# Kernel optimization log

Measured on AMD Instinct MI355X. Metric: run time of the kernel, lower is better.

Reference implementation:

```python
import jax, jax.numpy as jnp
import numpy as np

DIM = 1024
HEADS = 16
DIM_HEAD = 64
INNER = HEADS * DIM_HEAD
LN_EPS = 1e-5


def setup_inputs() -> dict:
    key = jax.random.key(0)
    ks = jax.random.split(key, 6)
    b, n = 2, 2048
    x = jax.random.normal(ks[0], (b, n, DIM), dtype=jnp.float32)
    attn_bias = jax.random.normal(ks[1], (HEADS, n, n), dtype=jnp.float32)
    # learned params
    ln_gamma = jnp.ones((DIM,), dtype=jnp.float32)
    ln_beta = jnp.zeros((DIM,), dtype=jnp.float32)
    w_qkv = jax.random.normal(ks[2], (DIM, 3 * INNER), dtype=jnp.float32) / np.sqrt(DIM)
    w_out = jax.random.normal(ks[3], (INNER, DIM), dtype=jnp.float32) / np.sqrt(INNER)
    return {"x": x, "attn_bias": attn_bias, "ln_gamma": ln_gamma,
            "ln_beta": ln_beta, "w_qkv": w_qkv, "w_out": w_out}


def reference(x, attn_bias, ln_gamma, ln_beta, w_qkv, w_out):
    b, n, _ = x.shape
    scale = DIM_HEAD ** -0.5
    # LayerNorm
    mu = jnp.mean(x, axis=-1, keepdims=True)
    var = jnp.mean(jnp.square(x - mu), axis=-1, keepdims=True)
    xn = (x - mu) * jax.lax.rsqrt(var + LN_EPS) * ln_gamma + ln_beta
    # QKV projection: [b, n, 3*inner]
    qkv = xn @ w_qkv
    q, k, v = jnp.split(qkv, 3, axis=-1)
    # [b, n, inner] -> [b, h, n, d]
    split_heads = lambda t: t.reshape(b, n, HEADS, DIM_HEAD).transpose(0, 2, 1, 3)
    q, k, v = split_heads(q) * scale, split_heads(k), split_heads(v)
    sim = jnp.einsum('bhid,bhjd->bhij', q, k)
    sim = sim + attn_bias[None]  # broadcast over batch
    mask_value = -jnp.finfo(sim.dtype).max
    causal = jnp.triu(jnp.ones((n, n), dtype=bool), k=1)
    sim = jnp.where(causal, mask_value, sim)
    attn = jax.nn.softmax(sim, axis=-1)
    out = jnp.einsum('bhij,bhjd->bhid', attn, v)
    out = out.transpose(0, 2, 1, 3).reshape(b, n, INNER)
    return out @ w_out
```

## Files before the change

kernel.cpp:

```cpp
#include <hip/hip_runtime.h>
#include <hip/hip_bf16.h>
#include <math.h>

typedef unsigned short u16;
typedef __attribute__((ext_vector_type(8))) __bf16 bf16x8;
typedef __attribute__((ext_vector_type(4))) float f32x4;

static __device__ __forceinline__ u16 f2bf(float f) {
    unsigned int u = __builtin_bit_cast(unsigned int, f);
    u += 0x7fffu + ((u >> 16) & 1u);
    return (u16)(u >> 16);
}

__global__ __launch_bounds__(256) void ln_kernel(
    const float* __restrict__ x, const float* __restrict__ g,
    const float* __restrict__ bta, u16* __restrict__ xn)
{
    const int row = blockIdx.x;
    const int tid = threadIdx.x;
    const float4 v = *(const float4*)&x[(size_t)row * 1024 + tid * 4];
    float s  = v.x + v.y + v.z + v.w;
    float s2 = v.x * v.x + v.y * v.y + v.z * v.z + v.w * v.w;
    #pragma unroll
    for (int off = 32; off; off >>= 1) {
        s  += __shfl_xor(s,  off);
        s2 += __shfl_xor(s2, off);
    }
    __shared__ float red[8];
    if ((tid & 63) == 0) { red[tid >> 6] = s; red[4 + (tid >> 6)] = s2; }
    __syncthreads();
    s  = red[0] + red[1] + red[2] + red[3];
    s2 = red[4] + red[5] + red[6] + red[7];
    const float mean = s * (1.0f / 1024.0f);
    const float var  = s2 * (1.0f / 1024.0f) - mean * mean;
    const float rstd = rsqrtf(var + 1e-5f);
    const float4 gg = *(const float4*)&g[tid * 4];
    const float4 bb = *(const float4*)&bta[tid * 4];
    ushort4 o;
    o.x = f2bf((v.x - mean) * rstd * gg.x + bb.x);
    o.y = f2bf((v.y - mean) * rstd * gg.y + bb.y);
    o.z = f2bf((v.z - mean) * rstd * gg.z + bb.z);
    o.w = f2bf((v.w - mean) * rstd * gg.w + bb.w);
    *(ushort4*)&xn[(size_t)row * 1024 + tid * 4] = o;
}

__global__ __launch_bounds__(256) void transpose_w(
    const float* __restrict__ in, u16* __restrict__ outT, int K, int N)
{
    const int k0 = blockIdx.x * 64, n0 = blockIdx.y * 64;
    const int tid = threadIdx.x;
    __shared__ u16 tile[64][72];
    #pragma unroll
    for (int i = 0; i < 4; ++i) {
        int c = tid + i * 256;
        int kr = c >> 4, nc = (c & 15) * 4;
        float4 v = *(const float4*)&in[(size_t)(k0 + kr) * N + n0 + nc];
        tile[nc + 0][kr] = f2bf(v.x);
        tile[nc + 1][kr] = f2bf(v.y);
        tile[nc + 2][kr] = f2bf(v.z);
        tile[nc + 3][kr] = f2bf(v.w);
    }
    __syncthreads();
    #pragma unroll
    for (int i = 0; i < 4; ++i) {
        int c = tid + i * 256;
        int nr = c >> 4, kc = (c & 15) * 4;
        ushort4 w = *(const ushort4*)&tile[nr][kc];
        *(ushort4*)&outT[(size_t)(n0 + nr) * K + k0 + kc] = w;
    }
}

__global__ __launch_bounds__(256) void transpose_v_kernel(
    const u16* __restrict__ V, u16* __restrict__ Vt)
{
    const int bh = blockIdx.y;
    const int n0 = blockIdx.x * 64;
    const int tid = threadIdx.x;
    __shared__ u16 t[64][72];
    #pragma unroll
    for (int i = 0; i < 2; ++i) {
        int c = tid + (i << 8);
        int nr = c >> 3, dc = (c & 7) * 8;
        int4 v4 = *(const int4*)&V[((size_t)bh * 2048 + n0 + nr) * 64 + dc];
        union { int4 v; u16 u[8]; } uu; uu.v = v4;
        #pragma unroll
        for (int j = 0; j < 8; ++j) t[dc + j][nr] = uu.u[j];
    }
    __syncthreads();
    #pragma unroll
    for (int i = 0; i < 2; ++i) {
        int c = tid + (i << 8);
        int d = c >> 3, nn = (c & 7) * 8;
        int4 v4 = *(const int4*)&t[d][nn];
        *(int4*)&Vt[((size_t)bh * 64 + d) * 2048 + n0 + nn] = v4;
    }
}

template <int EPI>
__global__ __launch_bounds__(256) void gemm_bf16_k(
    const u16* __restrict__ A, const u16* __restrict__ Bt,
    int M, int N, int K,
    float* __restrict__ Cf,
    u16* __restrict__ Qo, u16* __restrict__ Ko, u16* __restrict__ Vo)
{
    __shared__ u16 lds[2][8192];
    const int tid = threadIdx.x;
    const int lane = tid & 63, w = tid >> 6;
    const int l15 = lane & 15, l4 = lane >> 4;
    const int wm = w & 1, wn = w >> 1;
    const int n0 = blockIdx.x * 128, m0 = blockIdx.y * 128;

    auto stage = [&](int buf, int kt) {
        const u16* Ab = A + (size_t)m0 * K + kt * 32;
        const u16* Bb = Bt + (size_t)n0 * K + kt * 32;
        #pragma unroll
        for (int i = 0; i < 2; ++i) {
            int c = tid + (i << 8);
            int r = c >> 2, ke = (c & 3) * 8;
            __builtin_amdgcn_global_load_lds(
                (const __attribute__((address_space(1))) void*)(Ab + (size_t)r * K + ke),
                (__attribute__((address_space(3))) void*)(&lds[buf][0] + c * 8), 16, 0, 0);
            __builtin_amdgcn_global_load_lds(
                (const __attribute__((address_space(1))) void*)(Bb + (size_t)r * K + ke),
                (__attribute__((address_space(3))) void*)(&lds[buf][4096] + c * 8), 16, 0, 0);
        }
    };

    f32x4 acc[4][4];
    #pragma unroll
    for (int mf = 0; mf < 4; ++mf)
        #pragma unroll
        for (int nf = 0; nf < 4; ++nf)
            acc[mf][nf] = f32x4{0.f, 0.f, 0.f, 0.f};

    const int NT = K >> 5;
    stage(0, 0);
    __syncthreads();
    for (int kt = 0; kt < NT; ++kt) {
        const int buf = kt & 1;
        if (kt + 1 < NT) stage(buf ^ 1, kt + 1);
        const u16* Ab = &lds[buf][0];
        const u16* Bb = &lds[buf][4096];
        bf16x8 af[4], bfv[4];
        #pragma unroll
        for (int mf = 0; mf < 4; ++mf)
            af[mf] = *(const bf16x8*)(Ab + (wm * 64 + mf * 16 + l15) * 32 + l4 * 8);
        #pragma unroll
        for (int nf = 0; nf < 4; ++nf)
            bfv[nf] = *(const bf16x8*)(Bb + (wn * 64 + nf * 16 + l15) * 32 + l4 * 8);
        #pragma unroll
        for (int mf = 0; mf < 4; ++mf)
            #pragma unroll
            for (int nf = 0; nf < 4; ++nf)
                acc[mf][nf] = __builtin_amdgcn_mfma_f32_16x16x32_bf16(
                    af[mf], bfv[nf], acc[mf][nf], 0, 0, 0);
        __syncthreads();
    }

    #pragma unroll
    for (int mf = 0; mf < 4; ++mf) {
        #pragma unroll
        for (int nf = 0; nf < 4; ++nf) {
            #pragma unroll
            for (int r = 0; r < 4; ++r) {
                const int row = m0 + wm * 64 + mf * 16 + l4 * 4 + r;
                const int col = n0 + wn * 64 + nf * 16 + l15;
                const float v = acc[mf][nf][r];
                if (EPI == 1) {
                    Cf[(size_t)row * N + col] = v;
                } else {
                    const int t = col >> 10, rem = col & 1023;
                    const int h = rem >> 6, d = rem & 63;
                    const int b = row >> 11, nn = row & 2047;
                    const size_t idx = ((size_t)((b * 16 + h) * 2048 + nn)) * 64 + d;
                    if (t == 0)      Qo[idx] = f2bf(v * 0.125f);
                    else if (t == 1) Ko[idx] = f2bf(v);
                    else             Vo[idx] = f2bf(v);
                }
            }
        }
    }
}

__global__ __launch_bounds__(512, 4) void attn_kernel(
    const u16* __restrict__ Q, const u16* __restrict__ Kmat,
    const u16* __restrict__ Vt, const float* __restrict__ bias,
    u16* __restrict__ att)
{
    const int hb = blockIdx.x;
    const int h = hb >> 1, b = hb & 1;
    const int bh = b * 16 + h;
    const int y = blockIdx.y;
    const int qb = (y < 8) ? y : 23 - y;
    const int q0 = qb << 7;
    const int tid = threadIdx.x;
    const int w = tid >> 6, lane = tid & 63;
    const int l15 = lane & 15, l4 = lane >> 4;

    __shared__ u16 K_lds[2][64][76];
    __shared__ u16 V_lds[2][64][76];
    __shared__ u16 P_lds[8][16][76];

    const int qrow = q0 + w * 16 + l15;
    const int qlim = q0 + w * 16 + 15;

    bf16x8 qa[2];
    #pragma unroll
    for (int ks = 0; ks < 2; ++ks)
        qa[ks] = *(const bf16x8*)(Q + ((size_t)bh * 2048 + qrow) * 64 + ks * 32 + l4 * 8);

    f32x4 acc[4];
    #pragma unroll
    for (int nf = 0; nf < 4; ++nf) acc[nf] = f32x4{0.f, 0.f, 0.f, 0.f};
    float m_r = -INFINITY, l_r = 0.f;

    const float* biasq = bias + (size_t)h * 2048 * 2048 + (size_t)qrow * 2048;

    const int rr_s = tid >> 3, pp_s = (tid & 7) * 8;
    int4 kreg, vreg;
    auto issue_loads = [&](int j0n) {
        kreg = *(const int4*)&Kmat[((size_t)bh * 2048 + j0n + rr_s) * 64 + pp_s];
        vreg = *(const int4*)&Vt[((size_t)bh * 64 + rr_s) * 2048 + j0n + pp_s];
    };
    auto load_bias = [&](int j0n, float4 (&dst)[4]) {
        #pragma unroll
        for (int nf = 0; nf < 4; ++nf)
            dst[nf] = *(const float4*)&biasq[j0n + nf * 16 + l4 * 4];
    };

    const int NT = 2 * qb + 2;
    float4 bregA[4], bregB[4];

    issue_loads(0);
    load_bias(0, bregA);
    if (64 <= qlim && NT > 1) load_bias(64, bregB);

    auto tile_step = [&](int jt, float4 (&bcur)[4]) {
        const int j0 = jt << 6;
        const int buf = jt & 1;
        *(int4*)&K_lds[buf][rr_s][pp_s] = kreg;
        *(int4*)&V_lds[buf][rr_s][pp_s] = vreg;
        if (jt + 1 < NT) issue_loads((jt + 1) << 6);
        __builtin_amdgcn_sched_barrier(0);
        asm volatile("s_waitcnt lgkmcnt(0)" ::: "memory");
        __builtin_amdgcn_s_barrier();
        __builtin_amdgcn_sched_barrier(0);

        if (j0 <= qlim) {
            f32x4 s[4];
            #pragma unroll
            for (int nf = 0; nf < 4; ++nf) s[nf] = f32x4{0.f, 0.f, 0.f, 0.f};
            __builtin_amdgcn_s_setprio(1);
            #pragma unroll
            for (int ks = 0; ks < 2; ++ks)
                #pragma unroll
                for (int nf = 0; nf < 4; ++nf) {
                    bf16x8 kb = *(const bf16x8*)&K_lds[buf][nf * 16 + l15][ks * 32 + l4 * 8];
                    s[nf] = __builtin_amdgcn_mfma_f32_16x16x32_bf16(kb, qa[ks], s[nf], 0, 0, 0);
                }
            __builtin_amdgcn_s_setprio(0);

            if (j0 + 63 > q0 + w * 16) {
                #pragma unroll
                for (int nf = 0; nf < 4; ++nf) {
                    const int col0 = j0 + nf * 16 + l4 * 4;
                    #pragma unroll
                    for (int r = 0; r < 4; ++r) {
                        const float v = s[nf][r] + ((const float*)&bcur[nf])[r];
                        s[nf][r] = (col0 + r > qrow) ? -1e30f : v;
                    }
                }
            } else {
                #pragma unroll
                for (int nf = 0; nf < 4; ++nf)
                    #pragma unroll
                    for (int r = 0; r < 4; ++r)
                        s[nf][r] += ((const float*)&bcur[nf])[r];
            }
            if (jt + 2 < NT && ((jt + 2) << 6) <= qlim)
                load_bias((jt + 2) << 6, bcur);

            float mt = fmaxf(fmaxf(fmaxf(s[0][0], s[0][1]), fmaxf(s[0][2], s[0][3])),
                             fmaxf(fmaxf(s[1][0], s[1][1]), fmaxf(s[1][2], s[1][3])));
            mt = fmaxf(mt, fmaxf(fmaxf(fmaxf(s[2][0], s[2][1]), fmaxf(s[2][2], s[2][3])),
                                 fmaxf(fmaxf(s[3][0], s[3][1]), fmaxf(s[3][2], s[3][3]))));
            mt = fmaxf(mt, __shfl_xor(mt, 16));
            mt = fmaxf(mt, __shfl_xor(mt, 32));
            if (__any(mt > m_r + 8.0f)) {
                const float mn = fmaxf(m_r, mt);
                const float alpha = __expf(m_r - mn);
                m_r = mn;
                l_r *= alpha;
                #pragma unroll
                for (int nf = 0; nf < 4; ++nf)
                    #pragma unroll
                    for (int r = 0; r < 4; ++r) acc[nf][r] *= alpha;
            }

            float ps = 0.f;
            #pragma unroll
            for (int nf = 0; nf < 4; ++nf) {
                union { ushort4 v; u16 e[4]; } pw;
                #pragma unroll
                for (int r = 0; r < 4; ++r) {
                    const float e = __expf(s[nf][r] - m_r);
                    ps += e;
                    pw.e[r] = f2bf(e);
                }
                *(ushort4*)&P_lds[w][l15][nf * 16 + l4 * 4] = pw.v;
            }
            ps += __shfl_xor(ps, 16);
            ps += __shfl_xor(ps, 32);
            l_r += ps;

            __builtin_amdgcn_s_setprio(1);
            #pragma unroll
            for (int ks = 0; ks < 2; ++ks) {
                bf16x8 pa = *(const bf16x8*)&P_lds[w][l15][ks * 32 + l4 * 8];
                #pragma unroll
                for (int nf = 0; nf < 4; ++nf) {
                    bf16x8 vb = *(const bf16x8*)&V_lds[buf][nf * 16 + l15][ks * 32 + l4 * 8];
                    acc[nf] = __builtin_amdgcn_mfma_f32_16x16x32_bf16(vb, pa, acc[nf], 0, 0, 0);
                }
            }
            __builtin_amdgcn_s_setprio(0);
        }
    };

    for (int jt = 0; jt < NT; jt += 2) {
        tile_step(jt,     bregA);
        tile_step(jt + 1, bregB);
    }

    const float inv = 1.0f / l_r;
    #pragma unroll
    for (int nf = 0; nf < 4; ++nf) {
        union { ushort4 v; u16 e[4]; } o;
        #pragma unroll
        for (int r = 0; r < 4; ++r) o.e[r] = f2bf(acc[nf][r] * inv);
        *(ushort4*)&att[((size_t)b * 2048 + qrow) * 1024 + h * 64 + nf * 16 + l4 * 4] = o.v;
    }
}

extern "C" void kernel_launch(void* const* d_in, const int* in_sizes, int n_in,
                              void* d_out, int out_size, void* d_ws, size_t ws_size,
                              hipStream_t stream) {
    const float* x     = (const float*)d_in[0];
    const float* bias  = (const float*)d_in[1];
    const float* gamma = (const float*)d_in[2];
    const float* beta_ = (const float*)d_in[3];
    const float* wqkv  = (const float*)d_in[4];
    const float* wout  = (const float*)d_in[5];
    float* out = (float*)d_out;

    char* ws = (char*)d_ws;
    u16* xn     = (u16*)(ws + 0);
    u16* wqkvT  = (u16*)(ws + 8388608);
    u16* woutT  = (u16*)(ws + 14680064);
    u16* Qb     = (u16*)(ws + 16777216);
    u16* Kb     = (u16*)(ws + 25165824);
    u16* Vb     = (u16*)(ws + 33554432);
    u16* Vtb    = (u16*)(ws + 41943040);
    u16* attb   = xn;

    ln_kernel<<<4096, 256, 0, stream>>>(x, gamma, beta_, xn);
    transpose_w<<<dim3(16, 48), 256, 0, stream>>>(wqkv, wqkvT, 1024, 3072);
    transpose_w<<<dim3(16, 16), 256, 0, stream>>>(wout, woutT, 1024, 1024);
    gemm_bf16_k<0><<<dim3(24, 32), 256, 0, stream>>>(xn, wqkvT, 4096, 3072, 1024,
                                                     nullptr, Qb, Kb, Vb);
    transpose_v_kernel<<<dim3(32, 32), 256, 0, stream>>>(Vb, Vtb);
    attn_kernel<<<dim3(32, 16), 512, 0, stream>>>(Qb, Kb, Vtb, bias, attb);
    gemm_bf16_k<1><<<dim3(8, 32), 256, 0, stream>>>(attb, woutT, 4096, 1024, 1024,
                                                    out, nullptr, nullptr, nullptr);
}
```

Before: 151.5 us.

## Merge prep kernels, write V transposed from QKV GEMM, deepen K/V prefetch

Folds LayerNorm and both weight transposes into one prep kernel launch. The QKV GEMM epilogue now writes V directly in transposed layout as 4-element vector stores, which removes the separate V transpose kernel and its extra round trip through memory. The attention kernel double-buffers the K/V register prefetch two tiles ahead to hide more global load latency. The costs are more live registers in attention and strided scattered stores in the GEMM epilogue.

```diff
diff --git a/kernel.cpp b/kernel.cpp
--- a/kernel.cpp
+++ b/kernel.cpp
@@ -12,87 +12,65 @@
     return (u16)(u >> 16);
 }
 
-__global__ __launch_bounds__(256) void ln_kernel(
+__global__ __launch_bounds__(256) void prep_kernel(
     const float* __restrict__ x, const float* __restrict__ g,
-    const float* __restrict__ bta, u16* __restrict__ xn)
+    const float* __restrict__ bta, u16* __restrict__ xn,
+    const float* __restrict__ wqkv, u16* __restrict__ wqkvT,
+    const float* __restrict__ wout, u16* __restrict__ woutT)
 {
-    const int row = blockIdx.x;
+    const int bid = blockIdx.x;
     const int tid = threadIdx.x;
-    const float4 v = *(const float4*)&x[(size_t)row * 1024 + tid * 4];
-    float s  = v.x + v.y + v.z + v.w;
-    float s2 = v.x * v.x + v.y * v.y + v.z * v.z + v.w * v.w;
-    #pragma unroll
-    for (int off = 32; off; off >>= 1) {
-        s  += __shfl_xor(s,  off);
-        s2 += __shfl_xor(s2, off);
-    }
-    __shared__ float red[8];
-    if ((tid & 63) == 0) { red[tid >> 6] = s; red[4 + (tid >> 6)] = s2; }
-    __syncthreads();
-    s  = red[0] + red[1] + red[2] + red[3];
-    s2 = red[4] + red[5] + red[6] + red[7];
-    const float mean = s * (1.0f / 1024.0f);
-    const float var  = s2 * (1.0f / 1024.0f) - mean * mean;
-    const float rstd = rsqrtf(var + 1e-5f);
-    const float4 gg = *(const float4*)&g[tid * 4];
-    const float4 bb = *(const float4*)&bta[tid * 4];
-    ushort4 o;
-    o.x = f2bf((v.x - mean) * rstd * gg.x + bb.x);
-    o.y = f2bf((v.y - mean) * rstd * gg.y + bb.y);
-    o.z = f2bf((v.z - mean) * rstd * gg.z + bb.z);
-    o.w = f2bf((v.w - mean) * rstd * gg.w + bb.w);
-    *(ushort4*)&xn[(size_t)row * 1024 + tid * 4] = o;
-}
-
-__global__ __launch_bounds__(256) void transpose_w(
-    const float* __restrict__ in, u16* __restrict__ outT, int K, int N)
-{
-    const int k0 = blockIdx.x * 64, n0 = blockIdx.y * 64;
-    const int tid = threadIdx.x;
-    __shared__ u16 tile[64][72];
-    #pragma unroll
-    for (int i = 0; i < 4; ++i) {
-        int c = tid + i * 256;
-        int kr = c >> 4, nc = (c & 15) * 4;
-        float4 v = *(const float4*)&in[(size_t)(k0 + kr) * N + n0 + nc];
-        tile[nc + 0][kr] = f2bf(v.x);
-        tile[nc + 1][kr] = f2bf(v.y);
-        tile[nc + 2][kr] = f2bf(v.z);
-        tile[nc + 3][kr] = f2bf(v.w);
-    }
-    __syncthreads();
-    #pragma unroll
-    for (int i = 0; i < 4; ++i) {
-        int c = tid + i * 256;
-        int nr = c >> 4, kc = (c & 15) * 4;
-        ushort4 w = *(const ushort4*)&tile[nr][kc];
-        *(ushort4*)&outT[(size_t)(n0 + nr) * K + k0 + kc] = w;
-    }
-}
-
-__global__ __launch_bounds__(256) void transpose_v_kernel(
-    const u16* __restrict__ V, u16* __restrict__ Vt)
-{
-    const int bh = blockIdx.y;
-    const int n0 = blockIdx.x * 64;
-    const int tid = threadIdx.x;
-    __shared__ u16 t[64][72];
-    #pragma unroll
-    for (int i = 0; i < 2; ++i) {
-        int c = tid + (i << 8);
-        int nr = c >> 3, dc = (c & 7) * 8;
-        int4 v4 = *(const int4*)&V[((size_t)bh * 2048 + n0 + nr) * 64 + dc];
-        union { int4 v; u16 u[8]; } uu; uu.v = v4;
-        #pragma unroll
-        for (int j = 0; j < 8; ++j) t[dc + j][nr] = uu.u[j];
-    }
-    __syncthreads();
-    #pragma unroll
-    for (int i = 0; i < 2; ++i) {
-        int c = tid + (i << 8);
-        int d = c >> 3, nn = (c & 7) * 8;
-        int4 v4 = *(const int4*)&t[d][nn];
-        *(int4*)&Vt[((size_t)bh * 64 + d) * 2048 + n0 + nn] = v4;
+    if (bid < 4096) {
+        const int row = bid;
+        const float4 v = *(const float4*)&x[(size_t)row * 1024 + tid * 4];
+        float s  = v.x + v.y + v.z + v.w;
+        float s2 = v.x * v.x + v.y * v.y + v.z * v.z + v.w * v.w;
+        #pragma unroll
+        for (int off = 32; off; off >>= 1) {
+            s  += __shfl_xor(s,  off);
+            s2 += __shfl_xor(s2, off);
+        }
+        __shared__ float red[8];
+        if ((tid & 63) == 0) { red[tid >> 6] = s; red[4 + (tid >> 6)] = s2; }
+        __syncthreads();
+        s  = red[0] + red[1] + red[2] + red[3];
+        s2 = red[4] + red[5] + red[6] + red[7];
+        const float mean = s * (1.0f / 1024.0f);
+        const float var  = s2 * (1.0f / 1024.0f) - mean * mean;
+        const float rstd = rsqrtf(var + 1e-5f);
+        const float4 gg = *(const float4*)&g[tid * 4];
+        const float4 bb = *(const float4*)&bta[tid * 4];
+        ushort4 o;
+        o.x = f2bf((v.x - mean) * rstd * gg.x + bb.x);
+        o.y = f2bf((v.y - mean) * rstd * gg.y + bb.y);
+        o.z = f2bf((v.z - mean) * rstd * gg.z + bb.z);
+        o.w = f2bf((v.w - mean) * rstd * gg.w + bb.w);
+        *(ushort4*)&xn[(size_t)row * 1024 + tid * 4] = o;
+    } else {
+        const float* in; u16* outT; int N, idx;
+        if (bid < 4864) { in = wqkv; outT = wqkvT; N = 3072; idx = bid - 4096; }
+        else            { in = wout; outT = woutT; N = 1024; idx = bid - 4864; }
+        const int K = 1024;
+        const int k0 = (idx & 15) * 64, n0 = (idx >> 4) * 64;
+        __shared__ u16 tile[64][72];
+        #pragma unroll
+        for (int i = 0; i < 4; ++i) {
+            int c = tid + i * 256;
+            int kr = c >> 4, nc = (c & 15) * 4;
+            float4 v = *(const float4*)&in[(size_t)(k0 + kr) * N + n0 + nc];
+            tile[nc + 0][kr] = f2bf(v.x);
+            tile[nc + 1][kr] = f2bf(v.y);
+            tile[nc + 2][kr] = f2bf(v.z);
+            tile[nc + 3][kr] = f2bf(v.w);
+        }
+        __syncthreads();
+        #pragma unroll
+        for (int i = 0; i < 4; ++i) {
+            int c = tid + i * 256;
+            int nr = c >> 4, kc = (c & 15) * 4;
+            ushort4 w = *(const ushort4*)&tile[nr][kc];
+            *(ushort4*)&outT[(size_t)(n0 + nr) * K + k0 + kc] = w;
+        }
     }
 }
 
@@ -101,7 +79,7 @@
     const u16* __restrict__ A, const u16* __restrict__ Bt,
     int M, int N, int K,
     float* __restrict__ Cf,
-    u16* __restrict__ Qo, u16* __restrict__ Ko, u16* __restrict__ Vo)
+    u16* __restrict__ Qo, u16* __restrict__ Ko, u16* __restrict__ Vto)
 {
     __shared__ u16 lds[2][8192];
     const int tid = threadIdx.x;
@@ -161,21 +139,28 @@
     for (int mf = 0; mf < 4; ++mf) {
         #pragma unroll
         for (int nf = 0; nf < 4; ++nf) {
-            #pragma unroll
-            for (int r = 0; r < 4; ++r) {
-                const int row = m0 + wm * 64 + mf * 16 + l4 * 4 + r;
-                const int col = n0 + wn * 64 + nf * 16 + l15;
-                const float v = acc[mf][nf][r];
-                if (EPI == 1) {
-                    Cf[(size_t)row * N + col] = v;
+            const int row0 = m0 + wm * 64 + mf * 16 + l4 * 4;
+            const int col  = n0 + wn * 64 + nf * 16 + l15;
+            if (EPI == 1) {
+                #pragma unroll
+                for (int r = 0; r < 4; ++r)
+                    Cf[(size_t)(row0 + r) * N + col] = acc[mf][nf][r];
+            } else {
+                const int t = col >> 10, rem = col & 1023;
+                const int h = rem >> 6, d = rem & 63;
+                const int b0 = row0 >> 11, nn0 = row0 & 2047;
+                if (t == 2) {
+                    union { ushort4 v; u16 e[4]; } vv;
+                    #pragma unroll
+                    for (int r = 0; r < 4; ++r) vv.e[r] = f2bf(acc[mf][nf][r]);
+                    *(ushort4*)&Vto[((size_t)((b0 * 16 + h) * 64) + d) * 2048 + nn0] = vv.v;
                 } else {
-                    const int t = col >> 10, rem = col & 1023;
-                    const int h = rem >> 6, d = rem & 63;
-                    const int b = row >> 11, nn = row & 2047;
-                    const size_t idx = ((size_t)((b * 16 + h) * 2048 + nn)) * 64 + d;
-                    if (t == 0)      Qo[idx] = f2bf(v * 0.125f);
-                    else if (t == 1) Ko[idx] = f2bf(v);
-                    else             Vo[idx] = f2bf(v);
+                    #pragma unroll
+                    for (int r = 0; r < 4; ++r) {
+                        const size_t idx = ((size_t)((b0 * 16 + h) * 2048 + nn0 + r)) * 64 + d;
+                        if (t == 0) Qo[idx] = f2bf(acc[mf][nf][r] * 0.125f);
+                        else        Ko[idx] = f2bf(acc[mf][nf][r]);
+                    }
                 }
             }
         }
@@ -217,10 +202,9 @@
     const float* biasq = bias + (size_t)h * 2048 * 2048 + (size_t)qrow * 2048;
 
     const int rr_s = tid >> 3, pp_s = (tid & 7) * 8;
-    int4 kreg, vreg;
-    auto issue_loads = [&](int j0n) {
-        kreg = *(const int4*)&Kmat[((size_t)bh * 2048 + j0n + rr_s) * 64 + pp_s];
-        vreg = *(const int4*)&Vt[((size_t)bh * 64 + rr_s) * 2048 + j0n + pp_s];
+    auto issue_k = [&](int j0n, int4& kd, int4& vd) {
+        kd = *(const int4*)&Kmat[((size_t)bh * 2048 + j0n + rr_s) * 64 + pp_s];
+        vd = *(const int4*)&Vt[((size_t)bh * 64 + rr_s) * 2048 + j0n + pp_s];
     };
     auto load_bias = [&](int j0n, float4 (&dst)[4]) {
         #pragma unroll
@@ -229,18 +213,20 @@
     };
 
     const int NT = 2 * qb + 2;
+    int4 kA, vA, kB, vB;
     float4 bregA[4], bregB[4];
 
-    issue_loads(0);
+    issue_k(0, kA, vA);
+    issue_k(64, kB, vB);
     load_bias(0, bregA);
-    if (64 <= qlim && NT > 1) load_bias(64, bregB);
-
-    auto tile_step = [&](int jt, float4 (&bcur)[4]) {
+    if (64 <= qlim) load_bias(64, bregB);
+
+    auto tile_step = [&](int jt, int4& kcur, int4& vcur, float4 (&bcur)[4]) {
         const int j0 = jt << 6;
         const int buf = jt & 1;
-        *(int4*)&K_lds[buf][rr_s][pp_s] = kreg;
-        *(int4*)&V_lds[buf][rr_s][pp_s] = vreg;
-        if (jt + 1 < NT) issue_loads((jt + 1) << 6);
+        *(int4*)&K_lds[buf][rr_s][pp_s] = kcur;
+        *(int4*)&V_lds[buf][rr_s][pp_s] = vcur;
+        if (jt + 2 < NT) issue_k((jt + 2) << 6, kcur, vcur);
         __builtin_amdgcn_sched_barrier(0);
         asm volatile("s_waitcnt lgkmcnt(0)" ::: "memory");
         __builtin_amdgcn_s_barrier();
@@ -328,8 +314,8 @@
     };
 
     for (int jt = 0; jt < NT; jt += 2) {
-        tile_step(jt,     bregA);
-        tile_step(jt + 1, bregB);
+        tile_step(jt,     kA, vA, bregA);
+        tile_step(jt + 1, kB, vB, bregB);
     }
 
     const float inv = 1.0f / l_r;
@@ -359,16 +345,12 @@
     u16* woutT  = (u16*)(ws + 14680064);
     u16* Qb     = (u16*)(ws + 16777216);
     u16* Kb     = (u16*)(ws + 25165824);
-    u16* Vb     = (u16*)(ws + 33554432);
-    u16* Vtb    = (u16*)(ws + 41943040);
+    u16* Vtb    = (u16*)(ws + 33554432);
     u16* attb   = xn;
 
-    ln_kernel<<<4096, 256, 0, stream>>>(x, gamma, beta_, xn);
-    transpose_w<<<dim3(16, 48), 256, 0, stream>>>(wqkv, wqkvT, 1024, 3072);
-    transpose_w<<<dim3(16, 16), 256, 0, stream>>>(wout, woutT, 1024, 1024);
+    prep_kernel<<<5120, 256, 0, stream>>>(x, gamma, beta_, xn, wqkv, wqkvT, wout, woutT);
     gemm_bf16_k<0><<<dim3(24, 32), 256, 0, stream>>>(xn, wqkvT, 4096, 3072, 1024,
-                                                     nullptr, Qb, Kb, Vb);
-    transpose_v_kernel<<<dim3(32, 32), 256, 0, stream>>>(Vb, Vtb);
+                                                     nullptr, Qb, Kb, Vtb);
     attn_kernel<<<dim3(32, 16), 512, 0, stream>>>(Qb, Kb, Vtb, bias, attb);
     gemm_bf16_k<1><<<dim3(8, 32), 256, 0, stream>>>(attb, woutT, 4096, 1024, 1024,
                                                     out, nullptr, nullptr, nullptr);
```

Result: slower. 171.6 us (+13.3%).

## Merge LN and weight transposes into one launch; prefetch K/V two tiles ahead

Applied to the files above, without the earlier changes.

The LayerNorm and both weight transpose-casts now run as branches of a single prep kernel, removing two kernel launches and letting those independent jobs share the GPU. In the attention kernel, K and V global loads are double-buffered in registers and issued two tiles ahead instead of one, so memory latency has more time to hide behind compute. This raises register pressure in the attention kernel and adds LDS for the unused branch of the prep kernel.

```diff
diff --git a/kernel.cpp b/kernel.cpp
--- a/kernel.cpp
+++ b/kernel.cpp
@@ -12,61 +12,65 @@
     return (u16)(u >> 16);
 }
 
-__global__ __launch_bounds__(256) void ln_kernel(
+__global__ __launch_bounds__(256) void prep_kernel(
     const float* __restrict__ x, const float* __restrict__ g,
-    const float* __restrict__ bta, u16* __restrict__ xn)
+    const float* __restrict__ bta, u16* __restrict__ xn,
+    const float* __restrict__ wqkv, u16* __restrict__ wqkvT,
+    const float* __restrict__ wout, u16* __restrict__ woutT)
 {
-    const int row = blockIdx.x;
+    const int bid = blockIdx.x;
     const int tid = threadIdx.x;
-    const float4 v = *(const float4*)&x[(size_t)row * 1024 + tid * 4];
-    float s  = v.x + v.y + v.z + v.w;
-    float s2 = v.x * v.x + v.y * v.y + v.z * v.z + v.w * v.w;
-    #pragma unroll
-    for (int off = 32; off; off >>= 1) {
-        s  += __shfl_xor(s,  off);
-        s2 += __shfl_xor(s2, off);
-    }
-    __shared__ float red[8];
-    if ((tid & 63) == 0) { red[tid >> 6] = s; red[4 + (tid >> 6)] = s2; }
-    __syncthreads();
-    s  = red[0] + red[1] + red[2] + red[3];
-    s2 = red[4] + red[5] + red[6] + red[7];
-    const float mean = s * (1.0f / 1024.0f);
-    const float var  = s2 * (1.0f / 1024.0f) - mean * mean;
-    const float rstd = rsqrtf(var + 1e-5f);
-    const float4 gg = *(const float4*)&g[tid * 4];
-    const float4 bb = *(const float4*)&bta[tid * 4];
-    ushort4 o;
-    o.x = f2bf((v.x - mean) * rstd * gg.x + bb.x);
-    o.y = f2bf((v.y - mean) * rstd * gg.y + bb.y);
-    o.z = f2bf((v.z - mean) * rstd * gg.z + bb.z);
-    o.w = f2bf((v.w - mean) * rstd * gg.w + bb.w);
-    *(ushort4*)&xn[(size_t)row * 1024 + tid * 4] = o;
-}
-
-__global__ __launch_bounds__(256) void transpose_w(
-    const float* __restrict__ in, u16* __restrict__ outT, int K, int N)
-{
-    const int k0 = blockIdx.x * 64, n0 = blockIdx.y * 64;
-    const int tid = threadIdx.x;
-    __shared__ u16 tile[64][72];
-    #pragma unroll
-    for (int i = 0; i < 4; ++i) {
-        int c = tid + i * 256;
-        int kr = c >> 4, nc = (c & 15) * 4;
-        float4 v = *(const float4*)&in[(size_t)(k0 + kr) * N + n0 + nc];
-        tile[nc + 0][kr] = f2bf(v.x);
-        tile[nc + 1][kr] = f2bf(v.y);
-        tile[nc + 2][kr] = f2bf(v.z);
-        tile[nc + 3][kr] = f2bf(v.w);
-    }
-    __syncthreads();
-    #pragma unroll
-    for (int i = 0; i < 4; ++i) {
-        int c = tid + i * 256;
-        int nr = c >> 4, kc = (c & 15) * 4;
-        ushort4 w = *(const ushort4*)&tile[nr][kc];
-        *(ushort4*)&outT[(size_t)(n0 + nr) * K + k0 + kc] = w;
+    if (bid < 4096) {
+        const int row = bid;
+        const float4 v = *(const float4*)&x[(size_t)row * 1024 + tid * 4];
+        float s  = v.x + v.y + v.z + v.w;
+        float s2 = v.x * v.x + v.y * v.y + v.z * v.z + v.w * v.w;
+        #pragma unroll
+        for (int off = 32; off; off >>= 1) {
+            s  += __shfl_xor(s,  off);
+            s2 += __shfl_xor(s2, off);
+        }
+        __shared__ float red[8];
+        if ((tid & 63) == 0) { red[tid >> 6] = s; red[4 + (tid >> 6)] = s2; }
+        __syncthreads();
+        s  = red[0] + red[1] + red[2] + red[3];
+        s2 = red[4] + red[5] + red[6] + red[7];
+        const float mean = s * (1.0f / 1024.0f);
+        const float var  = s2 * (1.0f / 1024.0f) - mean * mean;
+        const float rstd = rsqrtf(var + 1e-5f);
+        const float4 gg = *(const float4*)&g[tid * 4];
+        const float4 bb = *(const float4*)&bta[tid * 4];
+        ushort4 o;
+        o.x = f2bf((v.x - mean) * rstd * gg.x + bb.x);
+        o.y = f2bf((v.y - mean) * rstd * gg.y + bb.y);
+        o.z = f2bf((v.z - mean) * rstd * gg.z + bb.z);
+        o.w = f2bf((v.w - mean) * rstd * gg.w + bb.w);
+        *(ushort4*)&xn[(size_t)row * 1024 + tid * 4] = o;
+    } else {
+        const float* in; u16* outT; int N, idx;
+        if (bid < 4864) { in = wqkv; outT = wqkvT; N = 3072; idx = bid - 4096; }
+        else            { in = wout; outT = woutT; N = 1024; idx = bid - 4864; }
+        const int K = 1024;
+        const int k0 = (idx & 15) * 64, n0 = (idx >> 4) * 64;
+        __shared__ u16 tile[64][72];
+        #pragma unroll
+        for (int i = 0; i < 4; ++i) {
+            int c = tid + i * 256;
+            int kr = c >> 4, nc = (c & 15) * 4;
+            float4 v = *(const float4*)&in[(size_t)(k0 + kr) * N + n0 + nc];
+            tile[nc + 0][kr] = f2bf(v.x);
+            tile[nc + 1][kr] = f2bf(v.y);
+            tile[nc + 2][kr] = f2bf(v.z);
+            tile[nc + 3][kr] = f2bf(v.w);
+        }
+        __syncthreads();
+        #pragma unroll
+        for (int i = 0; i < 4; ++i) {
+            int c = tid + i * 256;
+            int nr = c >> 4, kc = (c & 15) * 4;
+            ushort4 w = *(const ushort4*)&tile[nr][kc];
+            *(ushort4*)&outT[(size_t)(n0 + nr) * K + k0 + kc] = w;
+        }
     }
 }
 
@@ -217,10 +221,9 @@
     const float* biasq = bias + (size_t)h * 2048 * 2048 + (size_t)qrow * 2048;
 
     const int rr_s = tid >> 3, pp_s = (tid & 7) * 8;
-    int4 kreg, vreg;
-    auto issue_loads = [&](int j0n) {
-        kreg = *(const int4*)&Kmat[((size_t)bh * 2048 + j0n + rr_s) * 64 + pp_s];
-        vreg = *(const int4*)&Vt[((size_t)bh * 64 + rr_s) * 2048 + j0n + pp_s];
+    auto issue_k = [&](int j0n, int4& kd, int4& vd) {
+        kd = *(const int4*)&Kmat[((size_t)bh * 2048 + j0n + rr_s) * 64 + pp_s];
+        vd = *(const int4*)&Vt[((size_t)bh * 64 + rr_s) * 2048 + j0n + pp_s];
     };
     auto load_bias = [&](int j0n, float4 (&dst)[4]) {
         #pragma unroll
@@ -229,18 +232,20 @@
     };
 
     const int NT = 2 * qb + 2;
+    int4 kA, vA, kB, vB;
     float4 bregA[4], bregB[4];
 
-    issue_loads(0);
+    issue_k(0, kA, vA);
+    issue_k(64, kB, vB);
     load_bias(0, bregA);
-    if (64 <= qlim && NT > 1) load_bias(64, bregB);
-
-    auto tile_step = [&](int jt, float4 (&bcur)[4]) {
+    if (64 <= qlim) load_bias(64, bregB);
+
+    auto tile_step = [&](int jt, int4& kcur, int4& vcur, float4 (&bcur)[4]) {
         const int j0 = jt << 6;
         const int buf = jt & 1;
-        *(int4*)&K_lds[buf][rr_s][pp_s] = kreg;
-        *(int4*)&V_lds[buf][rr_s][pp_s] = vreg;
-        if (jt + 1 < NT) issue_loads((jt + 1) << 6);
+        *(int4*)&K_lds[buf][rr_s][pp_s] = kcur;
+        *(int4*)&V_lds[buf][rr_s][pp_s] = vcur;
+        if (jt + 2 < NT) issue_k((jt + 2) << 6, kcur, vcur);
         __builtin_amdgcn_sched_barrier(0);
         asm volatile("s_waitcnt lgkmcnt(0)" ::: "memory");
         __builtin_amdgcn_s_barrier();
@@ -328,8 +333,8 @@
     };
 
     for (int jt = 0; jt < NT; jt += 2) {
-        tile_step(jt,     bregA);
-        tile_step(jt + 1, bregB);
+        tile_step(jt,     kA, vA, bregA);
+        tile_step(jt + 1, kB, vB, bregB);
     }
 
     const float inv = 1.0f / l_r;
@@ -363,9 +368,7 @@
     u16* Vtb    = (u16*)(ws + 41943040);
     u16* attb   = xn;
 
-    ln_kernel<<<4096, 256, 0, stream>>>(x, gamma, beta_, xn);
-    transpose_w<<<dim3(16, 48), 256, 0, stream>>>(wqkv, wqkvT, 1024, 3072);
-    transpose_w<<<dim3(16, 16), 256, 0, stream>>>(wout, woutT, 1024, 1024);
+    prep_kernel<<<5120, 256, 0, stream>>>(x, gamma, beta_, xn, wqkv, wqkvT, wout, woutT);
     gemm_bf16_k<0><<<dim3(24, 32), 256, 0, stream>>>(xn, wqkvT, 4096, 3072, 1024,
                                                      nullptr, Qb, Kb, Vb);
     transpose_v_kernel<<<dim3(32, 32), 256, 0, stream>>>(Vb, Vtb);
```

After: 177.9 us. 17.4% more time.
